# Optimization experiments

Measured on AMD Instinct MI355X. Metric: run time of the kernel, lower is better.

The kernel has to match this reference:

```python
import jax, jax.numpy as jnp
import numpy as np

B, T, D = 4, 2048, 1024
H, HS = 16, 64  # num heads, head size; H*HS == D


def setup_inputs() -> dict:
    key = jax.random.key(0)
    ks = jax.random.split(key, 6)
    scale = D ** -0.5
    x = jax.random.normal(ks[0], (B, T, D), dtype=jnp.float32)
    # per-head projections, stacked: [H, D, HS]
    Wq = jax.random.normal(ks[1], (H, D, HS), dtype=jnp.float32) * scale
    Wk = jax.random.normal(ks[2], (H, D, HS), dtype=jnp.float32) * scale
    Wv = jax.random.normal(ks[3], (H, D, HS), dtype=jnp.float32) * scale
    # output projection: [H*HS, D] + bias [D]
    Wp = jax.random.normal(ks[4], (H * HS, D), dtype=jnp.float32) * ((H * HS) ** -0.5)
    bp = jax.random.normal(ks[5], (D,), dtype=jnp.float32) * 0.01
    return {"x": x, "Wq": Wq, "Wk": Wk, "Wv": Wv, "Wp": Wp, "bp": bp}


def reference(x, Wq, Wk, Wv, Wp, bp):
    # per-head Q, K, V projections (batched over heads): [B, H, T, HS]
    q = jnp.einsum('btd,hde->bhte', x, Wq)
    k = jnp.einsum('btd,hde->bhte', x, Wk)
    v = jnp.einsum('btd,hde->bhte', x, Wv)
    # scaled scores with causal mask: [B, H, T, T]
    scores = jnp.einsum('bhte,bhse->bhts', q, k) * (HS ** -0.5)
    causal = jnp.tril(jnp.ones((T, T), dtype=bool))
    scores = jnp.where(causal, scores, jnp.float32(-jnp.inf))
    wei = jax.nn.softmax(scores, axis=-1)  # dropout is identity at eval
    out = jnp.einsum('bhts,bhse->bhte', wei, v)
    # concat heads -> [B, T, H*HS], then output projection
    out = out.transpose(0, 2, 1, 3).reshape(B, T, H * HS)
    return out @ Wp + bp
```

## Files before the change

kernel.cpp:

```cpp
#include <hip/hip_runtime.h>
#include <stdint.h>

typedef __attribute__((ext_vector_type(8))) short short8;
typedef __attribute__((ext_vector_type(4))) float f32x4;
typedef __attribute__((ext_vector_type(16))) float f32x16;

__device__ __forceinline__ unsigned short f2bf(float f) {
  unsigned u = __float_as_uint(f);
  u = u + 0x7FFFu + ((u >> 16) & 1u);
  return (unsigned short)(u >> 16);
}
__device__ __forceinline__ unsigned cvtpk_bf16(float lo, float hi) {
  unsigned r;
  asm("v_cvt_pk_bf16_f32 %0, %1, %2" : "=v"(r) : "v"(lo), "v"(hi));
  return r;
}
__device__ __forceinline__ float fast_exp2(float x) {
#if __has_builtin(__builtin_amdgcn_exp2f)
  return __builtin_amdgcn_exp2f(x);
#else
  return exp2f(x);
#endif
}
__device__ __forceinline__ void gl2lds16(const void* g, void* l) {
  __builtin_amdgcn_global_load_lds(
      (const __attribute__((address_space(1))) void*)(uintptr_t)g,
      (__attribute__((address_space(3))) void*)(uintptr_t)l, 16, 0, 0);
}

__global__ __launch_bounds__(256) void pack_x_kernel(const float* __restrict__ x,
                                                     ushort* __restrict__ xb) {
  int i = (blockIdx.x * 256 + threadIdx.x) * 8;
  float4 a = *(const float4*)(x + i);
  float4 b = *(const float4*)(x + i + 4);
  uint4 o;
  o.x = (unsigned)f2bf(a.x) | ((unsigned)f2bf(a.y) << 16);
  o.y = (unsigned)f2bf(a.z) | ((unsigned)f2bf(a.w) << 16);
  o.z = (unsigned)f2bf(b.x) | ((unsigned)f2bf(b.y) << 16);
  o.w = (unsigned)f2bf(b.z) | ((unsigned)f2bf(b.w) << 16);
  *(uint4*)(xb + i) = o;
}

__global__ __launch_bounds__(256) void pack_w_kernel(const float* __restrict__ Wq,
                                                     const float* __restrict__ Wk,
                                                     const float* __restrict__ Wv,
                                                     const float* __restrict__ Wp,
                                                     ushort* __restrict__ WqkvT,
                                                     ushort* __restrict__ WpT) {
  __shared__ float tile[64][65];
  const int bid = blockIdx.x;
  const int tid = threadIdx.x;
  const int lr = tid >> 6;
  const int lc = tid & 63;
  if (bid < 768) {
    const int s = bid >> 8;
    const int rem = bid & 255;
    const int h = rem >> 4;
    const int dt = rem & 15;
    const float* W = (s == 0) ? Wq : (s == 1) ? Wk : Wv;
    const float scale = (s == 0) ? 0.18033688011f : 1.0f;
#pragma unroll
    for (int p = 0; p < 16; ++p) {
      int r = p * 4 + lr;
      tile[r][lc] = W[(size_t)(h * 1024 + dt * 64 + r) * 64 + lc];
    }
    __syncthreads();
#pragma unroll
    for (int p = 0; p < 16; ++p) {
      int e = p * 4 + lr;
      float v = tile[lc][e] * scale;
      WqkvT[(size_t)(s * 1024 + h * 64 + e) * 1024 + dt * 64 + lc] = f2bf(v);
    }
  } else {
    const int t = bid - 768;
    const int rt = t >> 4, ct = t & 15;
#pragma unroll
    for (int p = 0; p < 16; ++p) {
      int r = p * 4 + lr;
      tile[r][lc] = Wp[(size_t)(rt * 64 + r) * 1024 + ct * 64 + lc];
    }
    __syncthreads();
#pragma unroll
    for (int p = 0; p < 16; ++p) {
      int c = p * 4 + lr;
      float v = tile[lc][c];
      WpT[(size_t)(ct * 64 + c) * 1024 + rt * 64 + lc] = f2bf(v);
    }
  }
}

template <int OUT_MODE>
__global__ __launch_bounds__(256) void gemm_bt(const ushort* __restrict__ A,
                                               const ushort* __restrict__ BT,
                                               ushort* __restrict__ Cb,
                                               float* __restrict__ Cf,
                                               const float* __restrict__ bias,
                                               int M, int N, int K) {
  __shared__ __align__(16) ushort Al[128 * 32];
  __shared__ __align__(16) ushort Bl[128 * 32];
  const int tid = threadIdx.x;
  const int lane = tid & 63;
  const int wave = tid >> 6;
  const int wm = wave >> 1, wn = wave & 1;
  const int nbx = gridDim.x;
  const int nwg = nbx * gridDim.y;
  int wg = blockIdx.y * nbx + blockIdx.x;
  wg = (wg & 7) * (nwg >> 3) + (wg >> 3);
  const int m0 = (wg / nbx) * 128, n0 = (wg % nbx) * 128;
  const int r16 = lane & 15, g = lane >> 4;
  f32x4 acc[4][4] = {};
  const int kTiles = K >> 5;
  const size_t ldb = (size_t)K * 2;
  const int srow = tid >> 2;
  const int srb = (tid & 3) * 16;
  const char* a_src = (const char*)A + (size_t)(m0 + srow) * ldb + srb;
  const char* b_src = (const char*)BT + (size_t)(n0 + srow) * ldb + srb;
  char* a_dst = (char*)Al + wave * 1024;
  char* b_dst = (char*)Bl + wave * 1024;
  for (int kt = 0; kt < kTiles; ++kt) {
    const int k0b = kt * 64;
    if (kt) __syncthreads();
    gl2lds16(a_src + k0b, a_dst);
    gl2lds16(a_src + (size_t)64 * ldb + k0b, a_dst + 4096);
    gl2lds16(b_src + k0b, b_dst);
    gl2lds16(b_src + (size_t)64 * ldb + k0b, b_dst + 4096);
    __syncthreads();
    short8 af[4], bfr[4];
#pragma unroll
    for (int i = 0; i < 4; ++i) {
      af[i] = *(const short8*)(Al + ((wm * 64 + i * 16 + r16) * 32 + g * 8));
      bfr[i] = *(const short8*)(Bl + ((wn * 64 + i * 16 + r16) * 32 + g * 8));
    }
#pragma unroll
    for (int mi = 0; mi < 4; ++mi)
#pragma unroll
      for (int ni = 0; ni < 4; ++ni)
        acc[mi][ni] =
            __builtin_amdgcn_mfma_f32_16x16x32_bf16(af[mi], bfr[ni], acc[mi][ni], 0, 0, 0);
  }
#pragma unroll
  for (int mi = 0; mi < 4; ++mi)
#pragma unroll
    for (int ni = 0; ni < 4; ++ni)
#pragma unroll
      for (int r = 0; r < 4; ++r) {
        int row = m0 + wm * 64 + mi * 16 + g * 4 + r;
        int col = n0 + wn * 64 + ni * 16 + r16;
        float v = acc[mi][ni][r];
        if (OUT_MODE == 0) {
          Cb[(size_t)row * N + col] = f2bf(v);
        } else {
          Cf[(size_t)row * N + col] = v + bias[col];
        }
      }
}

__global__ __launch_bounds__(256) void attn_mfma_kernel(const ushort* __restrict__ QKV,
                                                        ushort* __restrict__ O) {
  int flat = blockIdx.z * 128 + blockIdx.y * 8 + blockIdx.x;
  flat = (flat & 7) * 64 + (flat >> 3);
  const int qtA = flat & 7;
  const int h = (flat >> 3) & 15;
  const int b = flat >> 7;
  __shared__ __align__(16) ushort Kl[64 * 64];
  __shared__ __align__(16) ushort VT[64 * 64];
  const int tid = threadIdx.x;
  const int lane = tid & 63;
  const int wave = tid >> 6;
  const int lo5 = lane & 31;
  const int hi = lane >> 5;

  const int k_key0 = wave * 16 + (lane >> 3);
  const int k_key1 = k_key0 + 8;
  const int ksrc_off0 = ((lane & 7) * 16) ^ ((k_key0 & 7) << 4);
  const int ksrc_off1 = ((lane & 7) * 16) ^ ((k_key1 & 7) << 4);
  const char* kgbase = (const char*)(QKV + ((size_t)b * 2048) * 3072 + 1024 + h * 64);
  const int kp2 = (tid & 31) * 2;
  const int dg = tid >> 5;
  const char* vgbase = (const char*)(QKV + ((size_t)b * 2048) * 3072 + 2048 + h * 64 + dg * 8);

#pragma unroll
  for (int ph = 0; ph < 2; ++ph) {
    const int qt = ph ? qtA : (15 - qtA);
    const int qbase = qt * 128 + wave * 32;
    const int qg = qbase + lo5;

    short8 qf[4];
    {
      const ushort* qp = QKV + ((size_t)(b * 2048 + qbase + lo5) * 3072) + h * 64 + hi * 8;
#pragma unroll
      for (int dc = 0; dc < 4; ++dc) qf[dc] = *(const short8*)(qp + dc * 16);
    }

    f32x16 o0 = {}, o1 = {};
    float l_acc = 0.f;
    const int nblk = qt * 2 + 2;

    uint4 nv0, nv1;
    {
      const char* vp = vgbase + (size_t)kp2 * 6144;
      nv0 = *(const uint4*)(vp);
      nv1 = *(const uint4*)(vp + 6144);
    }

    for (int blk = 0; blk < nblk; ++blk) {
      const int s0 = blk * 64;
      __syncthreads();
      {
        const ushort* e0 = (const ushort*)&nv0;
        const ushort* e1 = (const ushort*)&nv1;
#pragma unroll
        for (int j = 0; j < 8; ++j) {
          const int row = dg * 8 + j;
          *(unsigned*)((char*)VT + row * 128 + ((kp2 * 2) ^ ((row & 7) << 4))) =
              (unsigned)e0[j] | ((unsigned)e1[j] << 16);
        }
      }
      gl2lds16(kgbase + (size_t)(s0 + k_key0) * 6144 + ksrc_off0, (char*)Kl + wave * 2048);
      gl2lds16(kgbase + (size_t)(s0 + k_key1) * 6144 + ksrc_off1,
               (char*)Kl + wave * 2048 + 1024);
      __syncthreads();

      if (blk + 1 < nblk) {
        const char* vp = vgbase + (size_t)(s0 + 64 + kp2) * 6144;
        nv0 = *(const uint4*)(vp);
        nv1 = *(const uint4*)(vp + 6144);
      }

#pragma unroll
      for (int g2 = 0; g2 < 2; ++g2) {
        const int ks = s0 + g2 * 32;
        if (ks > qbase + 31) continue;
        f32x16 s_acc = {};
        const int krow = g2 * 32 + lo5;
        const char* ksrc = (const char*)Kl + krow * 128;
        const int ksw = (krow & 7) << 4;
#pragma unroll
        for (int dc = 0; dc < 4; ++dc) {
          short8 kf = *(const short8*)(ksrc + ((dc * 32 + hi * 16) ^ ksw));
          s_acc = __builtin_amdgcn_mfma_f32_32x32x16_bf16(kf, qf[dc], s_acc, 0, 0, 0);
        }
        float p[16];
        if (ks + 31 > qbase) {
          const int ksg = ks + 4 * hi;
#pragma unroll
          for (int r = 0; r < 16; ++r) {
            const int key_g = ksg + (r & 3) + 8 * (r >> 2);
            float pv = fast_exp2(s_acc[r]);
            pv = (key_g <= qg) ? pv : 0.f;
            p[r] = pv;
            l_acc += pv;
          }
        } else {
#pragma unroll
          for (int r = 0; r < 16; ++r) {
            float pv = fast_exp2(s_acc[r]);
            p[r] = pv;
            l_acc += pv;
          }
        }
#pragma unroll
        for (int kc = 0; kc < 2; ++kc) {
          unsigned w0 = cvtpk_bf16(p[kc * 8 + 0], p[kc * 8 + 1]);
          unsigned w2 = cvtpk_bf16(p[kc * 8 + 4], p[kc * 8 + 5]);
          unsigned w1 = cvtpk_bf16(p[kc * 8 + 2], p[kc * 8 + 3]);
          unsigned w3 = cvtpk_bf16(p[kc * 8 + 6], p[kc * 8 + 7]);
          asm("v_permlane32_swap_b32 %0, %1" : "+v"(w0), "+v"(w2));
          asm("v_permlane32_swap_b32 %0, %1" : "+v"(w1), "+v"(w3));
          uint4 paw;
          paw.x = w0; paw.y = w1; paw.z = w2; paw.w = w3;
          short8 pa = *(short8*)&paw;
          const int kb = (g2 * 32 + kc * 16 + hi * 8) * 2;
          {
            const int vrow = lo5;
            short8 vf =
                *(const short8*)((const char*)VT + vrow * 128 + (kb ^ ((vrow & 7) << 4)));
            o0 = __builtin_amdgcn_mfma_f32_32x32x16_bf16(pa, vf, o0, 0, 0, 0);
          }
          {
            const int vrow = 32 + lo5;
            short8 vf =
                *(const short8*)((const char*)VT + vrow * 128 + (kb ^ ((vrow & 7) << 4)));
            o1 = __builtin_amdgcn_mfma_f32_32x32x16_bf16(pa, vf, o1, 0, 0, 0);
          }
        }
      }
    }

    l_acc += __shfl_xor(l_acc, 32);
    const float linv = 1.f / l_acc;
#pragma unroll
    for (int r = 0; r < 16; ++r) {
      const int qr = (r & 3) + 8 * (r >> 2) + 4 * hi;
      const float li = __shfl(linv, qr);
      ushort* ob = O + ((size_t)(b * 2048 + qbase + qr) * 1024) + h * 64 + lo5;
      ob[0] = f2bf(o0[r] * li);
      ob[32] = f2bf(o1[r] * li);
    }
  }
}

extern "C" void kernel_launch(void* const* d_in, const int* in_sizes, int n_in,
                              void* d_out, int out_size, void* d_ws, size_t ws_size,
                              hipStream_t stream) {
  const float* x = (const float*)d_in[0];
  const float* Wq = (const float*)d_in[1];
  const float* Wk = (const float*)d_in[2];
  const float* Wv = (const float*)d_in[3];
  const float* Wp = (const float*)d_in[4];
  const float* bp = (const float*)d_in[5];
  float* out = (float*)d_out;

  ushort* xb = (ushort*)d_ws;
  ushort* WqkvT = xb + 8388608;
  ushort* WpT = WqkvT + 3145728;
  ushort* QKV = WpT + 1048576;
  ushort* O = QKV + 25165824;

  pack_x_kernel<<<4096, 256, 0, stream>>>(x, xb);
  pack_w_kernel<<<1024, 256, 0, stream>>>(Wq, Wk, Wv, Wp, WqkvT, WpT);
  gemm_bt<0><<<dim3(24, 64), 256, 0, stream>>>(xb, WqkvT, QKV, nullptr, nullptr,
                                               8192, 3072, 1024);
  attn_mfma_kernel<<<dim3(8, 16, 4), 256, 0, stream>>>(QKV, O);
  gemm_bt<1><<<dim3(8, 64), 256, 0, stream>>>(O, WpT, nullptr, out, bp,
                                              8192, 1024, 1024);
}
```

Before: 171.6 us.

## Triple-buffer GEMM loads, fuse pack kernels, compute softmax denominator via MFMA

The GEMM now keeps three LDS buffers, issues direct-to-LDS loads two k-tiles ahead, waits with explicit vmcnt and uses one barrier per iteration. It also XOR-swizzles the LDS layout to cut bank conflicts. The two pack kernels become one launch, saving a kernel launch. In attention, the row sums of P are computed with an extra MFMA against a ones vector instead of scalar adds and shuffles, which moves that work onto the matrix unit but sums the bf16-rounded P values.

```diff
diff --git a/kernel.cpp b/kernel.cpp
--- a/kernel.cpp
+++ b/kernel.cpp
@@ -28,28 +28,30 @@
       (__attribute__((address_space(3))) void*)(uintptr_t)l, 16, 0, 0);
 }
 
-__global__ __launch_bounds__(256) void pack_x_kernel(const float* __restrict__ x,
-                                                     ushort* __restrict__ xb) {
-  int i = (blockIdx.x * 256 + threadIdx.x) * 8;
-  float4 a = *(const float4*)(x + i);
-  float4 b = *(const float4*)(x + i + 4);
-  uint4 o;
-  o.x = (unsigned)f2bf(a.x) | ((unsigned)f2bf(a.y) << 16);
-  o.y = (unsigned)f2bf(a.z) | ((unsigned)f2bf(a.w) << 16);
-  o.z = (unsigned)f2bf(b.x) | ((unsigned)f2bf(b.y) << 16);
-  o.w = (unsigned)f2bf(b.z) | ((unsigned)f2bf(b.w) << 16);
-  *(uint4*)(xb + i) = o;
-}
-
-__global__ __launch_bounds__(256) void pack_w_kernel(const float* __restrict__ Wq,
-                                                     const float* __restrict__ Wk,
-                                                     const float* __restrict__ Wv,
-                                                     const float* __restrict__ Wp,
-                                                     ushort* __restrict__ WqkvT,
-                                                     ushort* __restrict__ WpT) {
+__global__ __launch_bounds__(256) void pack_all_kernel(const float* __restrict__ x,
+                                                       const float* __restrict__ Wq,
+                                                       const float* __restrict__ Wk,
+                                                       const float* __restrict__ Wv,
+                                                       const float* __restrict__ Wp,
+                                                       ushort* __restrict__ xb,
+                                                       ushort* __restrict__ WqkvT,
+                                                       ushort* __restrict__ WpT) {
   __shared__ float tile[64][65];
-  const int bid = blockIdx.x;
+  const int bid0 = blockIdx.x;
   const int tid = threadIdx.x;
+  if (bid0 < 4096) {
+    int i = (bid0 * 256 + tid) * 8;
+    float4 a = *(const float4*)(x + i);
+    float4 b = *(const float4*)(x + i + 4);
+    uint4 o;
+    o.x = (unsigned)f2bf(a.x) | ((unsigned)f2bf(a.y) << 16);
+    o.y = (unsigned)f2bf(a.z) | ((unsigned)f2bf(a.w) << 16);
+    o.z = (unsigned)f2bf(b.x) | ((unsigned)f2bf(b.y) << 16);
+    o.w = (unsigned)f2bf(b.z) | ((unsigned)f2bf(b.w) << 16);
+    *(uint4*)(xb + i) = o;
+    return;
+  }
+  const int bid = bid0 - 4096;
   const int lr = tid >> 6;
   const int lc = tid & 63;
   if (bid < 768) {
@@ -96,8 +98,8 @@
                                                float* __restrict__ Cf,
                                                const float* __restrict__ bias,
                                                int M, int N, int K) {
-  __shared__ __align__(16) ushort Al[128 * 32];
-  __shared__ __align__(16) ushort Bl[128 * 32];
+  __shared__ __align__(16) ushort Al[3][128 * 32];
+  __shared__ __align__(16) ushort Bl[3][128 * 32];
   const int tid = threadIdx.x;
   const int lane = tid & 63;
   const int wave = tid >> 6;
@@ -112,24 +114,39 @@
   const int kTiles = K >> 5;
   const size_t ldb = (size_t)K * 2;
   const int srow = tid >> 2;
-  const int srb = (tid & 3) * 16;
-  const char* a_src = (const char*)A + (size_t)(m0 + srow) * ldb + srb;
-  const char* b_src = (const char*)BT + (size_t)(n0 + srow) * ldb + srb;
-  char* a_dst = (char*)Al + wave * 1024;
-  char* b_dst = (char*)Bl + wave * 1024;
+  const int scolsw = ((tid & 3) * 16) ^ ((srow & 3) << 4);
+  const char* a_src = (const char*)A + (size_t)(m0 + srow) * ldb + scolsw;
+  const char* b_src = (const char*)BT + (size_t)(n0 + srow) * ldb + scolsw;
+  const size_t half = (size_t)64 * ldb;
+  char* a_d0 = (char*)&Al[0][0] + wave * 1024;
+  char* b_d0 = (char*)&Bl[0][0] + wave * 1024;
+
+#define STAGE(kt, slot)                                        \
+  {                                                            \
+    const int k0b = (kt) * 64;                                 \
+    gl2lds16(a_src + k0b, a_d0 + (slot)*8192);                 \
+    gl2lds16(a_src + half + k0b, a_d0 + (slot)*8192 + 4096);   \
+    gl2lds16(b_src + k0b, b_d0 + (slot)*8192);                 \
+    gl2lds16(b_src + half + k0b, b_d0 + (slot)*8192 + 4096);   \
+  }
+
+  STAGE(0, 0);
+  STAGE(1, 1);
+  asm volatile("s_waitcnt vmcnt(4)" ::: "memory");
+  __builtin_amdgcn_s_barrier();
+
+  int slot = 0;
+  const int swf = (r16 & 3) << 4;
   for (int kt = 0; kt < kTiles; ++kt) {
-    const int k0b = kt * 64;
-    if (kt) __syncthreads();
-    gl2lds16(a_src + k0b, a_dst);
-    gl2lds16(a_src + (size_t)64 * ldb + k0b, a_dst + 4096);
-    gl2lds16(b_src + k0b, b_dst);
-    gl2lds16(b_src + (size_t)64 * ldb + k0b, b_dst + 4096);
-    __syncthreads();
+    const int nslot = (slot == 0) ? 2 : slot - 1;
+    if (kt + 2 < kTiles) STAGE(kt + 2, nslot);
+    const char* Ab = (const char*)&Al[slot][0];
+    const char* Bb = (const char*)&Bl[slot][0];
     short8 af[4], bfr[4];
 #pragma unroll
     for (int i = 0; i < 4; ++i) {
-      af[i] = *(const short8*)(Al + ((wm * 64 + i * 16 + r16) * 32 + g * 8));
-      bfr[i] = *(const short8*)(Bl + ((wn * 64 + i * 16 + r16) * 32 + g * 8));
+      af[i] = *(const short8*)(Ab + (wm * 64 + i * 16 + r16) * 64 + ((g * 16) ^ swf));
+      bfr[i] = *(const short8*)(Bb + (wn * 64 + i * 16 + r16) * 64 + ((g * 16) ^ swf));
     }
 #pragma unroll
     for (int mi = 0; mi < 4; ++mi)
@@ -137,7 +154,16 @@
       for (int ni = 0; ni < 4; ++ni)
         acc[mi][ni] =
             __builtin_amdgcn_mfma_f32_16x16x32_bf16(af[mi], bfr[ni], acc[mi][ni], 0, 0, 0);
-  }
+    if (kt + 2 < kTiles) {
+      asm volatile("s_waitcnt vmcnt(4)" ::: "memory");
+    } else {
+      asm volatile("s_waitcnt vmcnt(0)" ::: "memory");
+    }
+    __builtin_amdgcn_s_barrier();
+    slot = (slot == 2) ? 0 : slot + 1;
+  }
+#undef STAGE
+
 #pragma unroll
   for (int mi = 0; mi < 4; ++mi)
 #pragma unroll
@@ -170,6 +196,10 @@
   const int lo5 = lane & 31;
   const int hi = lane >> 5;
 
+  short8 ones;
+#pragma unroll
+  for (int i = 0; i < 8; ++i) ones[i] = (short)0x3F80;
+
   const int k_key0 = wave * 16 + (lane >> 3);
   const int k_key1 = k_key0 + 8;
   const int ksrc_off0 = ((lane & 7) * 16) ^ ((k_key0 & 7) << 4);
@@ -192,8 +222,7 @@
       for (int dc = 0; dc < 4; ++dc) qf[dc] = *(const short8*)(qp + dc * 16);
     }
 
-    f32x16 o0 = {}, o1 = {};
-    float l_acc = 0.f;
+    f32x16 o0 = {}, o1 = {}, lacc = {};
     const int nblk = qt * 2 + 2;
 
     uint4 nv0, nv1;
@@ -247,17 +276,11 @@
           for (int r = 0; r < 16; ++r) {
             const int key_g = ksg + (r & 3) + 8 * (r >> 2);
             float pv = fast_exp2(s_acc[r]);
-            pv = (key_g <= qg) ? pv : 0.f;
-            p[r] = pv;
-            l_acc += pv;
+            p[r] = (key_g <= qg) ? pv : 0.f;
           }
         } else {
 #pragma unroll
-          for (int r = 0; r < 16; ++r) {
-            float pv = fast_exp2(s_acc[r]);
-            p[r] = pv;
-            l_acc += pv;
-          }
+          for (int r = 0; r < 16; ++r) p[r] = fast_exp2(s_acc[r]);
         }
 #pragma unroll
         for (int kc = 0; kc < 2; ++kc) {
@@ -271,6 +294,7 @@
           paw.x = w0; paw.y = w1; paw.z = w2; paw.w = w3;
           short8 pa = *(short8*)&paw;
           const int kb = (g2 * 32 + kc * 16 + hi * 8) * 2;
+          lacc = __builtin_amdgcn_mfma_f32_32x32x16_bf16(pa, ones, lacc, 0, 0, 0);
           {
             const int vrow = lo5;
             short8 vf =
@@ -287,12 +311,10 @@
       }
     }
 
-    l_acc += __shfl_xor(l_acc, 32);
-    const float linv = 1.f / l_acc;
 #pragma unroll
     for (int r = 0; r < 16; ++r) {
       const int qr = (r & 3) + 8 * (r >> 2) + 4 * hi;
-      const float li = __shfl(linv, qr);
+      const float li = 1.f / lacc[r];
       ushort* ob = O + ((size_t)(b * 2048 + qbase + qr) * 1024) + h * 64 + lo5;
       ob[0] = f2bf(o0[r] * li);
       ob[32] = f2bf(o1[r] * li);
@@ -317,8 +339,7 @@
   ushort* QKV = WpT + 1048576;
   ushort* O = QKV + 25165824;
 
-  pack_x_kernel<<<4096, 256, 0, stream>>>(x, xb);
-  pack_w_kernel<<<1024, 256, 0, stream>>>(Wq, Wk, Wv, Wp, WqkvT, WpT);
+  pack_all_kernel<<<5120, 256, 0, stream>>>(x, Wq, Wk, Wv, Wp, xb, WqkvT, WpT);
   gemm_bt<0><<<dim3(24, 64), 256, 0, stream>>>(xb, WqkvT, QKV, nullptr, nullptr,
                                                8192, 3072, 1024);
   attn_mfma_kernel<<<dim3(8, 16, 4), 256, 0, stream>>>(QKV, O);
```

Measured after the change: 166.9 us. -2.7%, faster.
